# Kernel tuning notes

Measured on AMD Instinct MI355X. Metric: run time of the kernel, lower is better.

The kernel has to match this reference:

```python
import jax, jax.numpy as jnp
import numpy as np

SEARCH_RANGE = 4  # matches args.search_range


def _displacements(r):
    # Exact channel ordering of the original double loop:
    # I=0 -> (0,0); then for i=1..r: (-i,0),(+i,0),(0,-i),(0,+i),
    # then for j=1..r: (-i,-j),(+i,+j),(-i,+j),(+i,-j).
    ds = [(0, 0)]
    for i in range(1, r + 1):
        ds += [(-i, 0), (i, 0), (0, -i), (0, i)]
        for j in range(1, r + 1):
            ds += [(-i, -j), (i, j), (-i, j), (i, -j)]
    return ds


def setup_inputs() -> dict:
    key = jax.random.key(0)
    k1, k2 = jax.random.split(key)
    B, C, H, W = 4, 128, 96, 160
    src = jax.random.normal(k1, (B, C, H, W), dtype=jnp.float32)
    tgt = jax.random.normal(k2, (B, C, H, W), dtype=jnp.float32)
    return {"src": src, "tgt": tgt}


def reference(src, tgt):
    r = SEARCH_RANGE
    B, C, H, W = src.shape
    D = (2 * r + 1) ** 2  # 81 displacement channels
    # Zero-pad tgt spatially so out-of-range shifted regions contribute 0,
    # matching the torch version's zero-initialized output slices.
    tgt_pad = jnp.pad(tgt, ((0, 0), (0, 0), (r, r), (r, r)))
    chans = []
    for dy, dx in _displacements(r):
        # shifted[b,c,y,x] = tgt[b,c,y+dy,x+dx] (0 outside)
        t = jax.lax.dynamic_slice(tgt_pad, (0, 0, r + dy, r + dx), (B, C, H, W))
        chans.append(jnp.einsum('bchw,bchw->bhw', src, t))
    out = jnp.stack(chans, axis=1)  # [B, D, H, W]
    return out / D
```

## Files before the change

kernel.cpp:

```cpp
#include <hip/hip_runtime.h>
#include <hip/hip_bf16.h>

#define BATCH 4
#define CHAN 128
#define HGT 96
#define WID 160
#define HW (HGT * WID)
#define THREADS 256

typedef __attribute__((ext_vector_type(8))) short short8;
typedef __attribute__((ext_vector_type(4))) float float4v;

__device__ __forceinline__ int chan_of(int dy, int dx) {
    if (dy == 0 && dx == 0) return 0;
    if (dx == 0) { int i = dy < 0 ? -dy : dy; return 1 + (i - 1) * 20 + (dy < 0 ? 0 : 1); }
    if (dy == 0) { int i = dx < 0 ? -dx : dx; return 1 + (i - 1) * 20 + (dx < 0 ? 2 : 3); }
    int i = dy < 0 ? -dy : dy;
    int j = dx < 0 ? -dx : dx;
    int s = (dy < 0) ? (dx < 0 ? 0 : 2) : (dx < 0 ? 3 : 1);
    return 1 + (i - 1) * 20 + 4 + (j - 1) * 4 + s;
}

__device__ __forceinline__ unsigned pk2(float a, float b) {
    __hip_bfloat162 h = __float22bfloat162_rn(make_float2(a, b));
    unsigned u;
    __builtin_memcpy(&u, &h, 4);
    return u;
}

union sl_u { uint4 v; short8 s; };

#define ST_DECODE(TAG, U)                                                     \
    const int oct##TAG = (U) & 15;                                            \
    const int u4##TAG  = (U) >> 4;                                            \
    const int row##TAG = (u4##TAG * 43) >> 8;        \
    const int xq##TAG  = u4##TAG - row##TAG * 6;                              \
    const int gr##TAG  = y0 + dy0 + row##TAG;                                 \
    const int gx##TAG  = x0 - 4 + xq##TAG * 4;               \
    const bool ok##TAG = ((unsigned)gr##TAG < (unsigned)HGT) &&               \
                         ((unsigned)gx##TAG < (unsigned)WID);                 \
    const int ga##TAG  = tb + (oct##TAG * 8 * HGT + gr##TAG) * WID + gx##TAG;

#define ST_ISSUE(TAG, COND)                                                   \
    _Pragma("unroll")                                                         \
    for (int j = 0; j < 8; ++j)                                               \
        p##TAG[j] = (COND) ? *(const float4v*)(tgt + ga##TAG + j * HW)        \
                           : (float4v){0.f, 0.f, 0.f, 0.f};

#define ST_WRITE(TAG)                                                         \
    _Pragma("unroll")                                                         \
    for (int i = 0; i < 4; ++i) {                                             \
        const int xl = xq##TAG * 4 + i;                                       \
        uint4 val;                                                            \
        val.x = pk2(p##TAG[0][i], p##TAG[1][i]);                              \
        val.y = pk2(p##TAG[2][i], p##TAG[3][i]);                              \
        val.z = pk2(p##TAG[4][i], p##TAG[5][i]);                              \
        val.w = pk2(p##TAG[6][i], p##TAG[7][i]);                              \
        s_b[(row##TAG * 24 + xl) * 16 + (oct##TAG ^ (xl & 15))] = val;        \
    }

__global__ __launch_bounds__(THREADS, 4)
void cost_volume_kernel(const float* __restrict__ src,
                        const float* __restrict__ tgt,
                        float* __restrict__ out) {
    __shared__ __align__(16) uint4 s_b[2432];
    __shared__ int s_tab[27];

    const int tid  = threadIdx.x;
    const int wv   = tid >> 6;
    const int lane = tid & 63;
    const int q    = lane >> 4;
    const int ln   = lane & 15;

    const int w    = blockIdx.x;
    const int slab = w & 7;
    const int b    = slab >> 1;
    const int yh   = slab & 1;
    const int r0   = w >> 3;
    const int dyg  = r0 % 3;
    const int t    = r0 / 3;
    const int x0   = (t % 10) * 16;
    const int y0   = yh * 48 + (t / 10) * 4;
    const int dy0  = dyg * 3 - 4;

    if (tid < 27) s_tab[tid] = chan_of(dy0 + tid / 9, tid % 9 - 4) * HW;

    const int tb = b * CHAN * HGT * WID;

    ST_DECODE(0, tid)
    ST_DECODE(1, tid + 256)
    ST_DECODE(2, tid + 512)
    const bool has2 = tid < 64;

    float4v p0[8], p1[8], p2[8];

    ST_ISSUE(0, ok0)

    const int y  = y0 + wv;
    const int sbase = (b * CHAN * HGT + y) * WID + x0 + ln + q * 8 * HW;
    float apay[32];
    #pragma unroll
    for (int ks = 0; ks < 4; ++ks)
        #pragma unroll
        for (int j = 0; j < 8; ++j)
            apay[ks * 8 + j] = src[sbase + (ks * 32 + j) * HW];

    ST_ISSUE(1, ok1)

    ST_WRITE(0)
    ST_ISSUE(2, has2 && ok2)
    short8 afr[4];
    #pragma unroll
    for (int ks = 0; ks < 4; ++ks) {
        sl_u f;
        f.v.x = pk2(apay[ks * 8 + 0], apay[ks * 8 + 1]);
        f.v.y = pk2(apay[ks * 8 + 2], apay[ks * 8 + 3]);
        f.v.z = pk2(apay[ks * 8 + 4], apay[ks * 8 + 5]);
        f.v.w = pk2(apay[ks * 8 + 6], apay[ks * 8 + 7]);
        afr[ks] = f.s;
    }
    ST_WRITE(1)
    if (has2) { ST_WRITE(2) }

    __syncthreads();

    const float inv = 1.0f / 81.0f;
    const int obase = (b * 81 * HGT + y) * WID + x0;
    #pragma unroll
    for (int dyi = 0; dyi < 3; ++dyi) {
        const int rr = wv + dyi;
        float4v a0 = (float4v){0.f, 0.f, 0.f, 0.f};
        float4v a1 = (float4v){0.f, 0.f, 0.f, 0.f};
        #pragma unroll
        for (int ks = 0; ks < 4; ++ks) {
            sl_u b0;
            b0.v = s_b[(rr * 24 + ln) * 16 + ((q + ks * 4) ^ ln)];
            a0 = __builtin_amdgcn_mfma_f32_16x16x32_bf16(afr[ks], b0.s, a0, 0, 0, 0);
        }
        #pragma unroll
        for (int ks = 0; ks < 4; ++ks) {
            sl_u b1;
            b1.v = s_b[(rr * 24 + 16 + ln) * 16 + ((q + ks * 4) ^ ln)];
            a1 = __builtin_amdgcn_mfma_f32_16x16x32_bf16(afr[ks], b1.s, a1, 0, 0, 0);
        }
        #pragma unroll
        for (int reg = 0; reg < 4; ++reg) {
            const int m = q * 4 + reg;
            const int t0x = ln - m;
            if ((unsigned)t0x <= 8u)
                out[obase + s_tab[dyi * 9 + t0x] + m] = a0[reg] * inv;
            const int t1x = ln + 16 - m;
            if ((unsigned)t1x <= 8u)
                out[obase + s_tab[dyi * 9 + t1x] + m] = a1[reg] * inv;
        }
    }
}

extern "C" void kernel_launch(void* const* d_in, const int* in_sizes, int n_in,
                              void* d_out, int out_size, void* d_ws, size_t ws_size,
                              hipStream_t stream) {
    const float* src = (const float*)d_in[0];
    const float* tgt = (const float*)d_in[1];
    float* out = (float*)d_out;
    cost_volume_kernel<<<dim3(2880, 1, 1), dim3(THREADS, 1, 1), 0, stream>>>(src, tgt, out);
}
```

Before: 136.6 us.

## Pre-convert inputs to NHWC bf16 in workspace, then stage tiles via global_load_lds

Adds a pre-pass kernel that transposes src and tgt into a channel-last bf16 layout stored in the workspace. The main MFMA kernel then reads contiguous 16-byte channel chunks, loading tgt tiles straight into LDS with global_load_lds and src fragments as short8 vectors. This removes the strided fp32 gathers and in-kernel bf16 packing that each block repeated for overlapping halo tiles. The cost is an extra launch plus a full read and write of both tensors. The original kernel stays as a fallback when the workspace is too small.

Result: faster. 120.2 us (-12.0%).

```diff
diff --git a/kernel.cpp b/kernel.cpp
--- a/kernel.cpp
+++ b/kernel.cpp
@@ -7,6 +7,8 @@
 #define WID 160
 #define HW (HGT * WID)
 #define THREADS 256
+#define TENSOR_ELEMS (BATCH * CHAN * HGT * WID)
+#define WS_NEED ((size_t)(2 * (size_t)TENSOR_ELEMS * 2))
 
 typedef __attribute__((ext_vector_type(8))) short short8;
 typedef __attribute__((ext_vector_type(4))) float float4v;
@@ -30,13 +32,144 @@
 
 union sl_u { uint4 v; short8 s; };
 
+__global__ __launch_bounds__(THREADS)
+void nhwc_bf16_kernel(const float* __restrict__ src,
+                      const float* __restrict__ tgt,
+                      ushort* __restrict__ ws) {
+    __shared__ unsigned s_t[64][65];
+    int r = blockIdx.x;
+    const int xb = r % 3; r /= 3;
+    const int y  = r % HGT; r /= HGT;
+    const int b  = r % BATCH; r /= BATCH;
+    const float* in = r ? tgt : src;
+    ushort* op0 = ws + (size_t)r * TENSOR_ELEMS;
+    const int x0 = xb * 64;
+    const int npx = (x0 + 64 <= WID) ? 64 : (WID - x0);
+
+    const int t  = threadIdx.x;
+    const int x1 = t & 63, cp0 = t >> 6;
+    if (x1 < npx) {
+        const int base = (b * CHAN * HGT + y) * WID + x0 + x1;
+        #pragma unroll
+        for (int i = 0; i < 16; ++i) {
+            const int cp = cp0 + i * 4;
+            float a = in[base + (2 * cp) * HW];
+            float c = in[base + (2 * cp + 1) * HW];
+            s_t[cp][x1] = pk2(a, c);
+        }
+    }
+    __syncthreads();
+    const int x2 = t >> 2, g = t & 3;
+    if (x2 < npx) {
+        ushort* op = op0 + ((size_t)(b * HGT + y) * WID + x0 + x2) * CHAN + g * 32;
+        #pragma unroll
+        for (int k = 0; k < 4; ++k) {
+            uint4 v;
+            v.x = s_t[g * 16 + k * 4 + 0][x2];
+            v.y = s_t[g * 16 + k * 4 + 1][x2];
+            v.z = s_t[g * 16 + k * 4 + 2][x2];
+            v.w = s_t[g * 16 + k * 4 + 3][x2];
+            *(uint4*)(op + k * 8) = v;
+        }
+    }
+}
+
+__global__ __launch_bounds__(THREADS)
+void cost_volume_mfma(const ushort* __restrict__ srcT,
+                      const ushort* __restrict__ tgtT,
+                      float* __restrict__ out) {
+    __shared__ __align__(16) uint4 s_b[2432];
+    __shared__ int s_tab[27];
+
+    const int tid  = threadIdx.x;
+    const int wv   = tid >> 6;
+    const int lane = tid & 63;
+    const int q    = lane >> 4;
+    const int ln   = lane & 15;
+
+    const int w    = blockIdx.x;
+    const int slab = w & 7;
+    const int b    = slab >> 1;
+    const int yh   = slab & 1;
+    const int r0   = w >> 3;
+    const int dyg  = r0 % 3;
+    const int t    = r0 / 3;
+    const int x0   = (t % 10) * 16;
+    const int y0   = yh * 48 + (t / 10) * 4;
+    const int dy0  = dyg * 3 - 4;
+
+    if (tid < 27) s_tab[tid] = chan_of(dy0 + tid / 9, tid % 9 - 4) * HW;
+
+    const ushort* tbase = tgtT + (size_t)b * HGT * WID * CHAN;
+    #pragma unroll
+    for (int k = 0; k < 9; ++k) {
+        const int u   = k * THREADS + tid;
+        const int j   = u & 15;
+        const int v16 = u >> 4;
+        const int row = v16 / 24;
+        const int x   = v16 - row * 24;
+        const int gr  = y0 + dy0 + row;
+        const int gx  = x0 - 4 + x;
+        const int oct = j ^ (x & 15);
+        unsigned* lp = (unsigned*)&s_b[k * THREADS + (tid & ~63)];
+        if (((unsigned)gr < (unsigned)HGT) && ((unsigned)gx < (unsigned)WID)) {
+            const unsigned* gp =
+                (const unsigned*)(tbase + ((gr * WID + gx) * CHAN + oct * 8));
+            __builtin_amdgcn_global_load_lds(gp, lp, 16, 0, 0);
+        } else {
+            s_b[u] = make_uint4(0u, 0u, 0u, 0u);
+        }
+    }
+
+    const int y = y0 + wv;
+    const ushort* abase =
+        srcT + ((size_t)(b * HGT + y) * WID + x0 + ln) * CHAN + q * 8;
+    short8 afr[4];
+    #pragma unroll
+    for (int ks = 0; ks < 4; ++ks)
+        afr[ks] = *(const short8*)(abase + ks * 32);
+
+    __syncthreads();
+
+    const float inv = 1.0f / 81.0f;
+    const int obase = (b * 81 * HGT + y) * WID + x0;
+    #pragma unroll
+    for (int dyi = 0; dyi < 3; ++dyi) {
+        const int rr = wv + dyi;
+        float4v a0 = (float4v){0.f, 0.f, 0.f, 0.f};
+        float4v a1 = (float4v){0.f, 0.f, 0.f, 0.f};
+        #pragma unroll
+        for (int ks = 0; ks < 4; ++ks) {
+            sl_u b0;
+            b0.v = s_b[(rr * 24 + ln) * 16 + ((q + ks * 4) ^ ln)];
+            a0 = __builtin_amdgcn_mfma_f32_16x16x32_bf16(afr[ks], b0.s, a0, 0, 0, 0);
+        }
+        #pragma unroll
+        for (int ks = 0; ks < 4; ++ks) {
+            sl_u b1;
+            b1.v = s_b[(rr * 24 + 16 + ln) * 16 + ((q + ks * 4) ^ ln)];
+            a1 = __builtin_amdgcn_mfma_f32_16x16x32_bf16(afr[ks], b1.s, a1, 0, 0, 0);
+        }
+        #pragma unroll
+        for (int reg = 0; reg < 4; ++reg) {
+            const int m = q * 4 + reg;
+            const int t0x = ln - m;
+            if ((unsigned)t0x <= 8u)
+                out[obase + s_tab[dyi * 9 + t0x] + m] = a0[reg] * inv;
+            const int t1x = ln + 16 - m;
+            if ((unsigned)t1x <= 8u)
+                out[obase + s_tab[dyi * 9 + t1x] + m] = a1[reg] * inv;
+        }
+    }
+}
+
 #define ST_DECODE(TAG, U)                                                     \
     const int oct##TAG = (U) & 15;                                            \
     const int u4##TAG  = (U) >> 4;                                            \
-    const int row##TAG = (u4##TAG * 43) >> 8;        \
+    const int row##TAG = (u4##TAG * 43) >> 8;                                 \
     const int xq##TAG  = u4##TAG - row##TAG * 6;                              \
     const int gr##TAG  = y0 + dy0 + row##TAG;                                 \
-    const int gx##TAG  = x0 - 4 + xq##TAG * 4;               \
+    const int gx##TAG  = x0 - 4 + xq##TAG * 4;                                \
     const bool ok##TAG = ((unsigned)gr##TAG < (unsigned)HGT) &&               \
                          ((unsigned)gx##TAG < (unsigned)WID);                 \
     const int ga##TAG  = tb + (oct##TAG * 8 * HGT + gr##TAG) * WID + gx##TAG;
@@ -60,9 +193,9 @@
     }
 
 __global__ __launch_bounds__(THREADS, 4)
-void cost_volume_kernel(const float* __restrict__ src,
-                        const float* __restrict__ tgt,
-                        float* __restrict__ out) {
+void cost_volume_fallback(const float* __restrict__ src,
+                          const float* __restrict__ tgt,
+                          float* __restrict__ out) {
     __shared__ __align__(16) uint4 s_b[2432];
     __shared__ int s_tab[27];
 
@@ -93,7 +226,6 @@
     const bool has2 = tid < 64;
 
     float4v p0[8], p1[8], p2[8];
-
     ST_ISSUE(0, ok0)
 
     const int y  = y0 + wv;
@@ -106,7 +238,6 @@
             apay[ks * 8 + j] = src[sbase + (ks * 32 + j) * HW];
 
     ST_ISSUE(1, ok1)
-
     ST_WRITE(0)
     ST_ISSUE(2, has2 && ok2)
     short8 afr[4];
@@ -162,5 +293,12 @@
     const float* src = (const float*)d_in[0];
     const float* tgt = (const float*)d_in[1];
     float* out = (float*)d_out;
-    cost_volume_kernel<<<dim3(2880, 1, 1), dim3(THREADS, 1, 1), 0, stream>>>(src, tgt, out);
-}
+    if (d_ws && ws_size >= WS_NEED) {
+        ushort* ws = (ushort*)d_ws;
+        nhwc_bf16_kernel<<<dim3(2304, 1, 1), dim3(THREADS, 1, 1), 0, stream>>>(src, tgt, ws);
+        cost_volume_mfma<<<dim3(2880, 1, 1), dim3(THREADS, 1, 1), 0, stream>>>(
+            ws, ws + TENSOR_ELEMS, out);
+    } else {
+        cost_volume_fallback<<<dim3(2880, 1, 1), dim3(THREADS, 1, 1), 0, stream>>>(src, tgt, out);
+    }
+}
```

## Fuse three dy-group blocks into one block and stage output through LDS

Applied to the files above, without the earlier changes.

Each block now handles all nine dy offsets for its 4x16 tile instead of three, using 512 threads split into two wave groups (4 and 5 dy rows). This removes the repeated src loads and the overlapping tgt halo loads that the 3x larger grid paid for. The MFMA results are written to shared memory and then stored to global memory as coalesced float4 rows, replacing scattered scalar stores. In exchange the grid drops to 960 blocks with a larger LDS footprint, which may reduce occupancy, and the two wave groups carry an uneven compute load.

New measurement: 116.7 us. 1.17x faster.

```diff
diff --git a/kernel.cpp b/kernel.cpp
--- a/kernel.cpp
+++ b/kernel.cpp
@@ -6,7 +6,7 @@
 #define HGT 96
 #define WID 160
 #define HW (HGT * WID)
-#define THREADS 256
+#define THREADS 512
 
 typedef __attribute__((ext_vector_type(8))) short short8;
 typedef __attribute__((ext_vector_type(4))) float float4v;
@@ -30,24 +30,25 @@
 
 union sl_u { uint4 v; short8 s; };
 
-#define ST_DECODE(TAG, U)                                                     \
-    const int oct##TAG = (U) & 15;                                            \
-    const int u4##TAG  = (U) >> 4;                                            \
-    const int row##TAG = (u4##TAG * 43) >> 8;        \
-    const int xq##TAG  = u4##TAG - row##TAG * 6;                              \
-    const int gr##TAG  = y0 + dy0 + row##TAG;                                 \
+#define FST_DECODE(TAG, U)                                                    \
+    const int u##TAG   = (U);                                                 \
+    const int xq##TAG  = u##TAG % 6;                                          \
+    const int r6##TAG  = u##TAG / 6;                              \
+    const int oct##TAG = r6##TAG & 15;                                        \
+    const int row##TAG = r6##TAG >> 4;                             \
+    const int gr##TAG  = y0 - 4 + row##TAG;                                   \
     const int gx##TAG  = x0 - 4 + xq##TAG * 4;               \
     const bool ok##TAG = ((unsigned)gr##TAG < (unsigned)HGT) &&               \
                          ((unsigned)gx##TAG < (unsigned)WID);                 \
     const int ga##TAG  = tb + (oct##TAG * 8 * HGT + gr##TAG) * WID + gx##TAG;
 
-#define ST_ISSUE(TAG, COND)                                                   \
+#define FST_ISSUE(TAG, COND)                                                  \
     _Pragma("unroll")                                                         \
     for (int j = 0; j < 8; ++j)                                               \
         p##TAG[j] = (COND) ? *(const float4v*)(tgt + ga##TAG + j * HW)        \
                            : (float4v){0.f, 0.f, 0.f, 0.f};
 
-#define ST_WRITE(TAG)                                                         \
+#define FST_WRITE(TAG)                                                        \
     _Pragma("unroll")                                                         \
     for (int i = 0; i < 4; ++i) {                                             \
         const int xl = xq##TAG * 4 + i;                                       \
@@ -59,15 +60,49 @@
         s_b[(row##TAG * 24 + xl) * 16 + (oct##TAG ^ (xl & 15))] = val;        \
     }
 
+#define COMPUTE_DY(DD, DYI)                                                   \
+    {                                                                         \
+        const int rr = wvy + (DYI);                                           \
+        float4v a0 = (float4v){0.f, 0.f, 0.f, 0.f};                           \
+        float4v a1 = (float4v){0.f, 0.f, 0.f, 0.f};                           \
+        _Pragma("unroll")                                                     \
+        for (int ks = 0; ks < 4; ++ks) {                                      \
+            sl_u b0;                                        \
+            b0.v = s_b[(rr * 24 + ln) * 16 + ((q + ks * 4) ^ ln)];            \
+            a0 = __builtin_amdgcn_mfma_f32_16x16x32_bf16(afr[ks], b0.s, a0, 0, 0, 0); \
+        }                                                                     \
+        _Pragma("unroll")                                                     \
+        for (int ks = 0; ks < 4; ++ks) {                                      \
+            sl_u b1;                                     \
+            b1.v = s_b[(rr * 24 + 16 + ln) * 16 + ((q + ks * 4) ^ ln)];       \
+            a1 = __builtin_amdgcn_mfma_f32_16x16x32_bf16(afr[ks], b1.s, a1, 0, 0, 0); \
+        }                                                                     \
+        aa0[DD] = a0; aa1[DD] = a1;                                           \
+    }
+
+#define EPI_DY(DD, DYI)                                                       \
+    _Pragma("unroll")                                                         \
+    for (int reg = 0; reg < 4; ++reg) {                                       \
+        const int m = q * 4 + reg;                                            \
+        const int t0x = ln - m;                            \
+        if ((unsigned)t0x <= 8u)                                              \
+            s_o[((DYI) * 9 + t0x) * 68 + wvy * 16 + m] = aa0[DD][reg] * inv;  \
+        const int t1x = ln + 16 - m;                       \
+        if ((unsigned)t1x <= 8u)                                              \
+            s_o[((DYI) * 9 + t1x) * 68 + wvy * 16 + m] = aa1[DD][reg] * inv;  \
+    }
+
 __global__ __launch_bounds__(THREADS, 4)
-void cost_volume_kernel(const float* __restrict__ src,
-                        const float* __restrict__ tgt,
-                        float* __restrict__ out) {
-    __shared__ __align__(16) uint4 s_b[2432];
-    __shared__ int s_tab[27];
+void cost_volume_fused(const float* __restrict__ src,
+                       const float* __restrict__ tgt,
+                       float* __restrict__ out) {
+    __shared__ __align__(16) uint4 s_b[4736];
+    __shared__ int s_tab[81];
 
     const int tid  = threadIdx.x;
     const int wv   = tid >> 6;
+    const int wvy  = wv & 3;
+    const int wvd  = wv >> 2;
     const int lane = tid & 63;
     const int q    = lane >> 4;
     const int ln   = lane & 15;
@@ -76,27 +111,24 @@
     const int slab = w & 7;
     const int b    = slab >> 1;
     const int yh   = slab & 1;
-    const int r0   = w >> 3;
-    const int dyg  = r0 % 3;
-    const int t    = r0 / 3;
+    const int t    = w >> 3;
     const int x0   = (t % 10) * 16;
     const int y0   = yh * 48 + (t / 10) * 4;
-    const int dy0  = dyg * 3 - 4;
-
-    if (tid < 27) s_tab[tid] = chan_of(dy0 + tid / 9, tid % 9 - 4) * HW;
+
+    if (tid < 81) s_tab[tid] = chan_of(tid / 9 - 4, tid % 9 - 4) * HW;
 
     const int tb = b * CHAN * HGT * WID;
 
-    ST_DECODE(0, tid)
-    ST_DECODE(1, tid + 256)
-    ST_DECODE(2, tid + 512)
-    const bool has2 = tid < 64;
+    FST_DECODE(0, tid)
+    FST_DECODE(1, tid + 512)
+    FST_DECODE(2, tid + 1024)
+    const bool has2 = tid < 128;
 
     float4v p0[8], p1[8], p2[8];
 
-    ST_ISSUE(0, ok0)
-
-    const int y  = y0 + wv;
+    FST_ISSUE(0, ok0)
+
+    const int y = y0 + wvy;
     const int sbase = (b * CHAN * HGT + y) * WID + x0 + ln + q * 8 * HW;
     float apay[32];
     #pragma unroll
@@ -105,10 +137,9 @@
         for (int j = 0; j < 8; ++j)
             apay[ks * 8 + j] = src[sbase + (ks * 32 + j) * HW];
 
-    ST_ISSUE(1, ok1)
-
-    ST_WRITE(0)
-    ST_ISSUE(2, has2 && ok2)
+    FST_ISSUE(1, ok1)
+    FST_WRITE(0)
+    FST_ISSUE(2, has2 && ok2)
     short8 afr[4];
     #pragma unroll
     for (int ks = 0; ks < 4; ++ks) {
@@ -119,39 +150,44 @@
         f.v.w = pk2(apay[ks * 8 + 6], apay[ks * 8 + 7]);
         afr[ks] = f.s;
     }
-    ST_WRITE(1)
-    if (has2) { ST_WRITE(2) }
+    FST_WRITE(1)
+    if (has2) { FST_WRITE(2) }
 
     __syncthreads();
 
+    float4v aa0[5], aa1[5];
+    if (wvd == 0) {
+        #pragma unroll
+        for (int dd = 0; dd < 4; ++dd) COMPUTE_DY(dd, dd)
+    } else {
+        #pragma unroll
+        for (int dd = 0; dd < 5; ++dd) COMPUTE_DY(dd, dd + 4)
+    }
+
+    __syncthreads();
+
+    float* s_o = (float*)s_b;
     const float inv = 1.0f / 81.0f;
-    const int obase = (b * 81 * HGT + y) * WID + x0;
+    if (wvd == 0) {
+        #pragma unroll
+        for (int dd = 0; dd < 4; ++dd) EPI_DY(dd, dd)
+    } else {
+        #pragma unroll
+        for (int dd = 0; dd < 5; ++dd) EPI_DY(dd, dd + 4)
+    }
+    __syncthreads();
+
+    const size_t ob = (size_t)b * 81 * HW + (size_t)y0 * WID + x0;
     #pragma unroll
-    for (int dyi = 0; dyi < 3; ++dyi) {
-        const int rr = wv + dyi;
-        float4v a0 = (float4v){0.f, 0.f, 0.f, 0.f};
-        float4v a1 = (float4v){0.f, 0.f, 0.f, 0.f};
-        #pragma unroll
-        for (int ks = 0; ks < 4; ++ks) {
-            sl_u b0;
-            b0.v = s_b[(rr * 24 + ln) * 16 + ((q + ks * 4) ^ ln)];
-            a0 = __builtin_amdgcn_mfma_f32_16x16x32_bf16(afr[ks], b0.s, a0, 0, 0, 0);
-        }
-        #pragma unroll
-        for (int ks = 0; ks < 4; ++ks) {
-            sl_u b1;
-            b1.v = s_b[(rr * 24 + 16 + ln) * 16 + ((q + ks * 4) ^ ln)];
-            a1 = __builtin_amdgcn_mfma_f32_16x16x32_bf16(afr[ks], b1.s, a1, 0, 0, 0);
-        }
-        #pragma unroll
-        for (int reg = 0; reg < 4; ++reg) {
-            const int m = q * 4 + reg;
-            const int t0x = ln - m;
-            if ((unsigned)t0x <= 8u)
-                out[obase + s_tab[dyi * 9 + t0x] + m] = a0[reg] * inv;
-            const int t1x = ln + 16 - m;
-            if ((unsigned)t1x <= 8u)
-                out[obase + s_tab[dyi * 9 + t1x] + m] = a1[reg] * inv;
+    for (int it = 0; it < 3; ++it) {
+        const int v = it * THREADS + tid;
+        if (v < 1296) {
+            const int xq  = v & 3;
+            const int row = v >> 2;
+            const int cix = row >> 2;
+            const int yy  = row & 3;
+            float4v val = *(const float4v*)&s_o[cix * 68 + yy * 16 + xq * 4];
+            *(float4v*)&out[ob + s_tab[cix] + yy * WID + xq * 4] = val;
         }
     }
 }
@@ -162,5 +198,5 @@
     const float* src = (const float*)d_in[0];
     const float* tgt = (const float*)d_in[1];
     float* out = (float*)d_out;
-    cost_volume_kernel<<<dim3(2880, 1, 1), dim3(THREADS, 1, 1), 0, stream>>>(src, tgt, out);
-}
+    cost_volume_fused<<<dim3(960, 1, 1), dim3(THREADS, 1, 1), 0, stream>>>(src, tgt, out);
+}
```
